# Optimization experiments

Measured on AMD Instinct MI355X. Metric: run time of the kernel, lower is better.

The kernel has to match this reference:

```python
import jax, jax.numpy as jnp
import numpy as np


def setup_inputs() -> dict:
    key = jax.random.key(0)
    kx, ky = jax.random.split(key)
    B, N, M = 32, 2048, 2048
    x = jax.random.normal(kx, (B, N, 3), dtype=jnp.float32)
    y = jax.random.normal(ky, (B, M, 3), dtype=jnp.float32)
    return {"x": x, "y": y}


def reference(x, y):
    # Faithful Chamfer distance matching the torch module.
    # Note: the original removes rows that sum exactly to 0; with random
    # float inputs no such rows exist, so that step is a no-op here.
    # d[b, i, j] = ||x[b, j] - y[b, i]||^2, shape [B, M, N]
    d = jnp.sum((x[:, None, :, :] - y[:, :, None, :]) ** 2, axis=-1)
    # min over y for each x point (dim 0 in the per-item [M, N] matrix)
    x_min = jnp.min(d, axis=1)  # [B, N]
    # min over x for each y point (dim 1)
    y_min = jnp.min(d, axis=2)  # [B, M]
    per_item = jnp.mean(x_min, axis=1) + jnp.mean(y_min, axis=1)  # [B]
    return jnp.mean(per_item)
```

## Files before the change

### kernel.cpp

```cpp
#include <hip/hip_runtime.h>


#define B_  32
#define N_  2048
#define PTS (B_ * N_)
#define ONEB 0x3F80u

typedef short  bf16x8 __attribute__((ext_vector_type(8)));
typedef float  f32x16 __attribute__((ext_vector_type(16)));

__device__ __forceinline__ unsigned short f2b(float f) {
    unsigned u = __float_as_uint(f);
    return (unsigned short)((u + 0x7FFFu + ((u >> 16) & 1u)) >> 16);
}
__device__ __forceinline__ float b2f(unsigned short h) {
    return __uint_as_float(((unsigned)h) << 16);
}
#define PK(a, b) (((unsigned)(a)) | (((unsigned)(b)) << 16))

__device__ __forceinline__ float min16(const f32x16 d) {
    const float a = fminf(fminf(d[0],  d[1]),  d[2]);
    const float b = fminf(fminf(d[3],  d[4]),  d[5]);
    const float c = fminf(fminf(d[6],  d[7]),  d[8]);
    const float e = fminf(fminf(d[9],  d[10]), d[11]);
    const float f = fminf(fminf(d[12], d[13]), d[14]);
    const float g = fminf(fminf(a, b), c);
    const float i = fminf(fminf(e, f), d[15]);
    return fminf(g, i);
}

__global__ __launch_bounds__(512, 4) void chamfer_mfma_kernel(
    const float* __restrict__ x, const float* __restrict__ y,
    float* __restrict__ partial)
{
    __shared__ unsigned sB[N_ * 8];
    __shared__ float pm[2][4][64];
    __shared__ float sred[4];

    const int bid  = blockIdx.x;
    const int dir  = bid >> 8;
    const int b    = (bid >> 3) & 31;
    const int qg   = bid & 7;
    const int tid  = threadIdx.x;
    const int lane = tid & 63;
    const int wv   = tid >> 6;
    const int qs2  = wv & 3;
    const int half = wv >> 2;
    const int h    = lane >> 5;
    const int ln31 = lane & 31;

    const float* q = dir ? y : x;
    const float* r = dir ? x : y;
    const float* rb = r + (size_t)b * N_ * 3;
    const float* qb = q + ((size_t)b * N_ + qg * 256 + qs2 * 64) * 3;

    for (int p = tid; p < N_; p += 512) {
        const float vx = rb[3 * p + 0], vy = rb[3 * p + 1], vz = rb[3 * p + 2];
        const unsigned short xh = f2b(vx), xl = f2b(vx - b2f(xh));
        const unsigned short yh = f2b(vy), yl = f2b(vy - b2f(yh));
        const unsigned short zh = f2b(vz), zl = f2b(vz - b2f(zh));
        const float nrm = fmaf(vx, vx, fmaf(vy, vy, vz * vz));
        const unsigned short nh = f2b(nrm), nl = f2b(nrm - b2f(nh));
        const unsigned base = ((unsigned)(p >> 5)) * 256u + ((unsigned)(p & 31)) * 4u;
        const uint4 lo = make_uint4(PK(xh, xl), PK(xh, xl), PK(yh, yl), PK(yh, yl));
        const uint4 hi = make_uint4(PK(zh, zl), PK(zh, zl), PK(nh, nl), PK(ONEB, ONEB));
        *(uint4*)(sB + base)        = lo;
        *(uint4*)(sB + base + 128)  = hi;
    }

    bf16x8 bq[2];
    #pragma unroll
    for (int s = 0; s < 2; ++s) {
        const float* qp = qb + (size_t)(s * 32 + ln31) * 3;
        const float vx = qp[0], vy = qp[1], vz = qp[2];
        const unsigned short xh = f2b(vx), xl = f2b(vx - b2f(xh));
        const unsigned short yh = f2b(vy), yl = f2b(vy - b2f(yh));
        const unsigned short zh = f2b(vz), zl = f2b(vz - b2f(zh));
        const float nrm = fmaf(vx, vx, fmaf(vy, vy, vz * vz));
        const unsigned short nh = f2b(nrm), nl = f2b(nrm - b2f(nh));
        const unsigned short mxh = f2b(-2.0f * b2f(xh)), mxl = f2b(-2.0f * b2f(xl));
        const unsigned short myh = f2b(-2.0f * b2f(yh)), myl = f2b(-2.0f * b2f(yl));
        const unsigned short mzh = f2b(-2.0f * b2f(zh)), mzl = f2b(-2.0f * b2f(zl));
        unsigned u[4];
        if (h == 0) {
            u[0] = PK(mxh, mxh); u[1] = PK(mxl, mxl);
            u[2] = PK(myh, myh); u[3] = PK(myl, myl);
        } else {
            u[0] = PK(mzh, mzh); u[1] = PK(mzl, mzl);
            u[2] = PK(ONEB, ONEB); u[3] = PK(nh, nl);
        }
        bq[s] = *(bf16x8*)u;
    }
    __syncthreads();

    const f32x16 zacc = {};
    float mac00 = 3.4e38f, mac01 = 3.4e38f;
    float mac10 = 3.4e38f, mac11 = 3.4e38f;
    const unsigned roff = (unsigned)h * 128u + (unsigned)ln31 * 4u;
    const unsigned* sBh = sB + half * 32 * 256;

    #pragma unroll 2
    for (int t = 0; t < 32; ++t) {
        const bf16x8 af = *(const bf16x8*)(sBh + t * 256 + roff);
        const f32x16 d0 = __builtin_amdgcn_mfma_f32_32x32x16_bf16(af, bq[0], zacc, 0, 0, 0);
        const f32x16 d1 = __builtin_amdgcn_mfma_f32_32x32x16_bf16(af, bq[1], zacc, 0, 0, 0);
        if (t & 1) { mac01 = fminf(mac01, min16(d0)); mac11 = fminf(mac11, min16(d1)); }
        else       { mac00 = fminf(mac00, min16(d0)); mac10 = fminf(mac10, min16(d1)); }
    }

    float m0 = fminf(mac00, mac01);
    float m1 = fminf(mac10, mac11);
    m0 = fminf(m0, __shfl_xor(m0, 32));
    m1 = fminf(m1, __shfl_xor(m1, 32));
    if (lane < 32) {
        pm[half][qs2][ln31]      = m0;
        pm[half][qs2][32 + ln31] = m1;
    }
    __syncthreads();

    if (tid < 256) {
        const float v = fminf(pm[0][tid >> 6][tid & 63],
                              pm[1][tid >> 6][tid & 63]);
        float s = v;
        s += __shfl_xor(s, 1);
        s += __shfl_xor(s, 2);
        s += __shfl_xor(s, 4);
        s += __shfl_xor(s, 8);
        s += __shfl_xor(s, 16);
        s += __shfl_xor(s, 32);
        if (lane == 0) sred[tid >> 6] = s;
    }
    __syncthreads();
    if (tid == 0) partial[bid] = (sred[0] + sred[1]) + (sred[2] + sred[3]);
}

__global__ __launch_bounds__(256) void chamfer_final_kernel(
    const float* __restrict__ partial, float* __restrict__ out)
{
    const int tid = threadIdx.x;
    float s = partial[tid] + partial[tid + 256];
    #pragma unroll
    for (int off = 32; off > 0; off >>= 1) s += __shfl_down(s, off);
    __shared__ float sr[4];
    if ((tid & 63) == 0) sr[tid >> 6] = s;
    __syncthreads();
    if (tid == 0)
        out[0] = ((sr[0] + sr[1]) + (sr[2] + sr[3])) * (1.0f / (float)PTS);
}

extern "C" void kernel_launch(void* const* d_in, const int* in_sizes, int n_in,
                              void* d_out, int out_size, void* d_ws, size_t ws_size,
                              hipStream_t stream)
{
    const float* x = (const float*)d_in[0];
    const float* y = (const float*)d_in[1];
    float* partial = (float*)d_ws;
    float* out     = (float*)d_out;

    chamfer_mfma_kernel<<<512, 512, 0, stream>>>(x, y, partial);
    chamfer_final_kernel<<<1, 256, 0, stream>>>(partial, out);
}
```

Baseline: 16.94 us.

## Split reference set across two blocks and add two-stage min/sum reduction

Each block now processes half of the reference points, so twice as many blocks (1024) are launched, each with half the shared memory, and occupancy is raised via launch bounds. Per-query partial minima are written to global memory and combined by a new reduction kernel that takes the min over the two halves and sums, followed by a final sum kernel. This is meant to improve load balance and CU occupancy across the GPU, at the cost of an extra kernel launch and global traffic for the partial minima.

```diff
diff --git a/kernel.cpp b/kernel.cpp
--- a/kernel.cpp
+++ b/kernel.cpp
@@ -29,18 +29,18 @@
     return fminf(g, i);
 }
 
-__global__ __launch_bounds__(512, 4) void chamfer_mfma_kernel(
+__global__ __launch_bounds__(512, 8) void chamfer_mfma_kernel(
     const float* __restrict__ x, const float* __restrict__ y,
-    float* __restrict__ partial)
+    float* __restrict__ partialm)
 {
-    __shared__ unsigned sB[N_ * 8];
+    __shared__ unsigned sB[1024 * 8];
     __shared__ float pm[2][4][64];
-    __shared__ float sred[4];
 
     const int bid  = blockIdx.x;
-    const int dir  = bid >> 8;
-    const int b    = (bid >> 3) & 31;
-    const int qg   = bid & 7;
+    const int dir  = bid >> 9;
+    const int b    = (bid >> 4) & 31;
+    const int qg   = (bid >> 1) & 7;
+    const int rh   = bid & 1;
     const int tid  = threadIdx.x;
     const int lane = tid & 63;
     const int wv   = tid >> 6;
@@ -51,10 +51,10 @@
 
     const float* q = dir ? y : x;
     const float* r = dir ? x : y;
-    const float* rb = r + (size_t)b * N_ * 3;
+    const float* rb = r + ((size_t)b * N_ + rh * 1024) * 3;
     const float* qb = q + ((size_t)b * N_ + qg * 256 + qs2 * 64) * 3;
 
-    for (int p = tid; p < N_; p += 512) {
+    for (int p = tid; p < 1024; p += 512) {
         const float vx = rb[3 * p + 0], vy = rb[3 * p + 1], vz = rb[3 * p + 2];
         const unsigned short xh = f2b(vx), xl = f2b(vx - b2f(xh));
         const unsigned short yh = f2b(vy), yl = f2b(vy - b2f(yh));
@@ -97,10 +97,10 @@
     float mac00 = 3.4e38f, mac01 = 3.4e38f;
     float mac10 = 3.4e38f, mac11 = 3.4e38f;
     const unsigned roff = (unsigned)h * 128u + (unsigned)ln31 * 4u;
-    const unsigned* sBh = sB + half * 32 * 256;
+    const unsigned* sBh = sB + half * 16 * 256;
 
     #pragma unroll 2
-    for (int t = 0; t < 32; ++t) {
+    for (int t = 0; t < 16; ++t) {
         const bf16x8 af = *(const bf16x8*)(sBh + t * 256 + roff);
         const f32x16 d0 = __builtin_amdgcn_mfma_f32_32x32x16_bf16(af, bq[0], zacc, 0, 0, 0);
         const f32x16 d1 = __builtin_amdgcn_mfma_f32_32x32x16_bf16(af, bq[1], zacc, 0, 0, 0);
@@ -121,31 +121,40 @@
     if (tid < 256) {
         const float v = fminf(pm[0][tid >> 6][tid & 63],
                               pm[1][tid >> 6][tid & 63]);
-        float s = v;
-        s += __shfl_xor(s, 1);
-        s += __shfl_xor(s, 2);
-        s += __shfl_xor(s, 4);
-        s += __shfl_xor(s, 8);
-        s += __shfl_xor(s, 16);
-        s += __shfl_xor(s, 32);
-        if (lane == 0) sred[tid >> 6] = s;
+        partialm[(size_t)bid * 256 + tid] = v;
     }
-    __syncthreads();
-    if (tid == 0) partial[bid] = (sred[0] + sred[1]) + (sred[2] + sred[3]);
 }
 
-__global__ __launch_bounds__(256) void chamfer_final_kernel(
-    const float* __restrict__ partial, float* __restrict__ out)
+__global__ __launch_bounds__(256) void chamfer_red1_kernel(
+    const float* __restrict__ partialm, float* __restrict__ part)
 {
     const int tid = threadIdx.x;
-    float s = partial[tid] + partial[tid + 256];
+    const int g4  = blockIdx.x * 1024 + tid * 4;
+    const int base = g4 >> 8;
+    const int qoff = g4 & 255;
+    const float4 v0 = *(const float4*)(partialm + ((size_t)base * 2 + 0) * 256 + qoff);
+    const float4 v1 = *(const float4*)(partialm + ((size_t)base * 2 + 1) * 256 + qoff);
+    float s = fminf(v0.x, v1.x) + fminf(v0.y, v1.y) +
+              fminf(v0.z, v1.z) + fminf(v0.w, v1.w);
     #pragma unroll
     for (int off = 32; off > 0; off >>= 1) s += __shfl_down(s, off);
     __shared__ float sr[4];
     if ((tid & 63) == 0) sr[tid >> 6] = s;
     __syncthreads();
-    if (tid == 0)
-        out[0] = ((sr[0] + sr[1]) + (sr[2] + sr[3])) * (1.0f / (float)PTS);
+    if (tid == 0) part[blockIdx.x] = (sr[0] + sr[1]) + (sr[2] + sr[3]);
+}
+
+__global__ __launch_bounds__(128) void chamfer_red2_kernel(
+    const float* __restrict__ part, float* __restrict__ out)
+{
+    const int tid = threadIdx.x;
+    float s = part[tid];
+    #pragma unroll
+    for (int off = 32; off > 0; off >>= 1) s += __shfl_down(s, off);
+    __shared__ float sr[2];
+    if ((tid & 63) == 0) sr[tid >> 6] = s;
+    __syncthreads();
+    if (tid == 0) out[0] = (sr[0] + sr[1]) * (1.0f / (float)PTS);
 }
 
 extern "C" void kernel_launch(void* const* d_in, const int* in_sizes, int n_in,
@@ -154,9 +163,12 @@
 {
     const float* x = (const float*)d_in[0];
     const float* y = (const float*)d_in[1];
-    float* partial = (float*)d_ws;
-    float* out     = (float*)d_out;
+    char* ws = (char*)d_ws;
+    float* partialm = (float*)ws;
+    float* part     = (float*)(ws + (size_t)2 * 1024 * 1024);
+    float* out      = (float*)d_out;
 
-    chamfer_mfma_kernel<<<512, 512, 0, stream>>>(x, y, partial);
-    chamfer_final_kernel<<<1, 256, 0, stream>>>(partial, out);
+    chamfer_mfma_kernel<<<1024, 512, 0, stream>>>(x, y, partialm);
+    chamfer_red1_kernel<<<128, 256, 0, stream>>>(partialm, part);
+    chamfer_red2_kernel<<<1, 128, 0, stream>>>(part, out);
 }
```

New measurement: 19.20 us. 1.13x slower.

## Swap MFMA work split: waves hold reference tiles, stream query fragments from LDS

Applied to the files above, without the earlier changes.

Each wave now keeps 8 reference-point A fragments in registers and loops over 8 query fragments staged in shared memory, instead of keeping 2 query fragments and streaming 32 reference tiles. Element-wise min across MFMA outputs happens before the horizontal min16 reduction, so there is one reduction per group of 8 MFMAs rather than one per MFMA. This aims to cut VALU min work and LDS reads per MFMA. In exchange the final reduction crosses 8 waves, shared-memory use and register pressure grow, and occupancy may drop.

```diff
diff --git a/kernel.cpp b/kernel.cpp
--- a/kernel.cpp
+++ b/kernel.cpp
@@ -34,7 +34,8 @@
     float* __restrict__ partial)
 {
     __shared__ unsigned sB[N_ * 8];
-    __shared__ float pm[2][4][64];
+    __shared__ unsigned sQ[2 * 1024];
+    __shared__ float pm[8][256];
     __shared__ float sred[4];
 
     const int bid  = blockIdx.x;
@@ -44,15 +45,13 @@
     const int tid  = threadIdx.x;
     const int lane = tid & 63;
     const int wv   = tid >> 6;
-    const int qs2  = wv & 3;
-    const int half = wv >> 2;
     const int h    = lane >> 5;
     const int ln31 = lane & 31;
 
     const float* q = dir ? y : x;
     const float* r = dir ? x : y;
     const float* rb = r + (size_t)b * N_ * 3;
-    const float* qb = q + ((size_t)b * N_ + qg * 256 + qs2 * 64) * 3;
+    const float* qb = q + ((size_t)b * N_ + qg * 256) * 3;
 
     for (int p = tid; p < N_; p += 512) {
         const float vx = rb[3 * p + 0], vy = rb[3 * p + 1], vz = rb[3 * p + 2];
@@ -68,10 +67,8 @@
         *(uint4*)(sB + base + 128)  = hi;
     }
 
-    bf16x8 bq[2];
-    #pragma unroll
-    for (int s = 0; s < 2; ++s) {
-        const float* qp = qb + (size_t)(s * 32 + ln31) * 3;
+    if (tid < 256) {
+        const float* qp = qb + (size_t)tid * 3;
         const float vx = qp[0], vy = qp[1], vz = qp[2];
         const unsigned short xh = f2b(vx), xl = f2b(vx - b2f(xh));
         const unsigned short yh = f2b(vy), yl = f2b(vy - b2f(yh));
@@ -81,46 +78,43 @@
         const unsigned short mxh = f2b(-2.0f * b2f(xh)), mxl = f2b(-2.0f * b2f(xl));
         const unsigned short myh = f2b(-2.0f * b2f(yh)), myl = f2b(-2.0f * b2f(yl));
         const unsigned short mzh = f2b(-2.0f * b2f(zh)), mzl = f2b(-2.0f * b2f(zl));
-        unsigned u[4];
-        if (h == 0) {
-            u[0] = PK(mxh, mxh); u[1] = PK(mxl, mxl);
-            u[2] = PK(myh, myh); u[3] = PK(myl, myl);
-        } else {
-            u[0] = PK(mzh, mzh); u[1] = PK(mzl, mzl);
-            u[2] = PK(ONEB, ONEB); u[3] = PK(nh, nl);
-        }
-        bq[s] = *(bf16x8*)u;
+        *(uint4*)(sQ + tid * 4) =
+            make_uint4(PK(mxh, mxh), PK(mxl, mxl), PK(myh, myh), PK(myl, myl));
+        *(uint4*)(sQ + 1024 + tid * 4) =
+            make_uint4(PK(mzh, mzh), PK(mzl, mzl), PK(ONEB, ONEB), PK(nh, nl));
     }
     __syncthreads();
 
+    const unsigned roff = (unsigned)h * 128u + (unsigned)ln31 * 4u;
+    bf16x8 af[8];
+    #pragma unroll
+    for (int j = 0; j < 8; ++j)
+        af[j] = *(const bf16x8*)(sB + (wv * 8 + j) * 256 + roff);
+
     const f32x16 zacc = {};
-    float mac00 = 3.4e38f, mac01 = 3.4e38f;
-    float mac10 = 3.4e38f, mac11 = 3.4e38f;
-    const unsigned roff = (unsigned)h * 128u + (unsigned)ln31 * 4u;
-    const unsigned* sBh = sB + half * 32 * 256;
-
-    #pragma unroll 2
-    for (int t = 0; t < 32; ++t) {
-        const bf16x8 af = *(const bf16x8*)(sBh + t * 256 + roff);
-        const f32x16 d0 = __builtin_amdgcn_mfma_f32_32x32x16_bf16(af, bq[0], zacc, 0, 0, 0);
-        const f32x16 d1 = __builtin_amdgcn_mfma_f32_32x32x16_bf16(af, bq[1], zacc, 0, 0, 0);
-        if (t & 1) { mac01 = fminf(mac01, min16(d0)); mac11 = fminf(mac11, min16(d1)); }
-        else       { mac00 = fminf(mac00, min16(d0)); mac10 = fminf(mac10, min16(d1)); }
-    }
-
-    float m0 = fminf(mac00, mac01);
-    float m1 = fminf(mac10, mac11);
-    m0 = fminf(m0, __shfl_xor(m0, 32));
-    m1 = fminf(m1, __shfl_xor(m1, 32));
-    if (lane < 32) {
-        pm[half][qs2][ln31]      = m0;
-        pm[half][qs2][32 + ln31] = m1;
+    const unsigned qroff = (unsigned)h * 1024u + (unsigned)ln31 * 4u;
+    #pragma unroll
+    for (int f = 0; f < 8; ++f) {
+        const bf16x8 bq = *(const bf16x8*)(sQ + qroff + f * 128);
+        f32x16 macc0 = __builtin_amdgcn_mfma_f32_32x32x16_bf16(af[0], bq, zacc, 0, 0, 0);
+        f32x16 macc1 = __builtin_amdgcn_mfma_f32_32x32x16_bf16(af[1], bq, zacc, 0, 0, 0);
+        #pragma unroll
+        for (int j = 2; j < 8; j += 2) {
+            const f32x16 d0 = __builtin_amdgcn_mfma_f32_32x32x16_bf16(af[j],     bq, zacc, 0, 0, 0);
+            const f32x16 d1 = __builtin_amdgcn_mfma_f32_32x32x16_bf16(af[j + 1], bq, zacc, 0, 0, 0);
+            macc0 = __builtin_elementwise_min(macc0, d0);
+            macc1 = __builtin_elementwise_min(macc1, d1);
+        }
+        float m = min16(__builtin_elementwise_min(macc0, macc1));
+        m = fminf(m, __shfl_xor(m, 32));
+        if (lane < 32) pm[wv][f * 32 + ln31] = m;
     }
     __syncthreads();
 
     if (tid < 256) {
-        const float v = fminf(pm[0][tid >> 6][tid & 63],
-                              pm[1][tid >> 6][tid & 63]);
+        float v = pm[0][tid];
+        #pragma unroll
+        for (int w = 1; w < 8; ++w) v = fminf(v, pm[w][tid]);
         float s = v;
         s += __shfl_xor(s, 1);
         s += __shfl_xor(s, 2);
```

After: 20.13 us. 18.8% more time.
